# Optimization experiments

Hardware: AMD Instinct MI355X
Metric: run time of the kernel (lower is better)

## Reference

```python
import jax, jax.numpy as jnp
import numpy as np

N = 50000
E = 800000
NODE_SIZE = 64
NUM_RADIAL = 20
CUTOFF = 5.0


def setup_inputs() -> dict:
    key = jax.random.key(0)
    ks = jax.random.split(key, 12)
    node_scalar = jax.random.normal(ks[0], (N, NODE_SIZE), dtype=jnp.float32)
    node_vector = jax.random.normal(ks[1], (N, 3, NODE_SIZE), dtype=jnp.float32)
    edge = jax.random.randint(ks[2], (E, 2), 0, N, dtype=jnp.int64)
    edge_diff = jax.random.normal(ks[3], (E, 3), dtype=jnp.float32)
    # positive distances in (0, cutoff]; most edges inside cutoff
    edge_dist = jax.random.uniform(ks[4], (E, 1), dtype=jnp.float32) * CUTOFF + 1e-2
    s = 1.0 / np.sqrt(NODE_SIZE)
    r = 1.0 / np.sqrt(NUM_RADIAL)
    W1 = jax.random.normal(ks[5], (NODE_SIZE, NODE_SIZE), dtype=jnp.float32) * s
    b1 = jnp.zeros((NODE_SIZE,), dtype=jnp.float32)
    W2 = jax.random.normal(ks[6], (NODE_SIZE, 3 * NODE_SIZE), dtype=jnp.float32) * s
    b2 = jnp.zeros((3 * NODE_SIZE,), dtype=jnp.float32)
    Wf = jax.random.normal(ks[7], (NUM_RADIAL, 3 * NODE_SIZE), dtype=jnp.float32) * r
    bf = jnp.zeros((3 * NODE_SIZE,), dtype=jnp.float32)
    return {"node_scalar": node_scalar, "node_vector": node_vector, "edge": edge,
            "edge_diff": edge_diff, "edge_dist": edge_dist,
            "W1": W1, "b1": b1, "W2": W2, "b2": b2, "Wf": Wf, "bf": bf}


def reference(node_scalar, node_vector, edge, edge_diff, edge_dist, W1, b1, W2, b2, Wf, bf):
    S = NODE_SIZE
    n_nodes = node_scalar.shape[0]
    # sinc radial basis: sin(n*pi*d/cutoff)/d, n=1..num_radial -> [E, R]
    n = jnp.arange(1, NUM_RADIAL + 1, dtype=edge_dist.dtype)
    rbf = jnp.sin(edge_dist * n * jnp.pi / CUTOFF) / edge_dist
    filter_weight = rbf @ Wf + bf                       # [E, 3S]
    # cosine cutoff, broadcast [E,1] over [E,3S]
    cut = jnp.where(edge_dist < CUTOFF,
                    0.5 * (jnp.cos(jnp.pi * edge_dist / CUTOFF) + 1.0),
                    jnp.zeros((), edge_dist.dtype))
    filter_weight = filter_weight * cut
    # scalar message MLP on nodes: Linear -> SiLU -> Linear
    scalar_out = jax.nn.silu(node_scalar @ W1 + b1) @ W2 + b2   # [N, 3S]
    src = edge[:, 1]
    dst = edge[:, 0]
    filter_out = filter_weight * scalar_out[src]        # [E, 3S]
    gate_state_vector = filter_out[:, :S]
    gate_edge_vector = filter_out[:, S:2 * S]
    message_scalar = filter_out[:, 2 * S:]
    unit = (edge_diff / edge_dist)[:, :, None]          # [E, 3, 1]
    message_vector = node_vector[src] * gate_state_vector[:, None, :] + gate_edge_vector[:, None, :] * unit  # [E,3,S]
    residual_scalar = jax.ops.segment_sum(message_scalar, dst, num_segments=n_nodes)
    residual_vector = jax.ops.segment_sum(message_vector, dst, num_segments=n_nodes)
    return node_scalar + residual_scalar, node_vector + residual_vector
```

## Files before the change

### kernel.cpp

```cpp
#include <hip/hip_runtime.h>
#include <hip/hip_bf16.h>
#include <math.h>

#define N_NODES 50000
#define N_EDGES 800000
#define NRAD 20
#define NBLK 196
#define CAP 48
#define NGRP 64
#define GSZ 782

typedef short bf16x8 __attribute__((ext_vector_type(8)));
typedef _Float16 f16x8 __attribute__((ext_vector_type(8)));
typedef float f32x4 __attribute__((ext_vector_type(4)));
typedef int i32x4 __attribute__((ext_vector_type(4)));
typedef int i32x2 __attribute__((ext_vector_type(2)));

__device__ __forceinline__ unsigned short f2b(float f) {
    union { __hip_bfloat16 h; unsigned short u; } cv;
    cv.h = __float2bfloat16(f);
    return cv.u;
}
__device__ __forceinline__ unsigned int packh2(float a, float b) {
    union { _Float16 h; unsigned short u; } A, B;
    A.h = (_Float16)a; B.h = (_Float16)b;
    return (unsigned int)A.u | ((unsigned int)B.u << 16);
}
__device__ __forceinline__ f32x4 mfma16(bf16x8 a, bf16x8 b, f32x4 c) {
    return __builtin_amdgcn_mfma_f32_16x16x32_bf16(a, b, c, 0, 0, 0);
}
__device__ __forceinline__ f32x4 mfma16h(f16x8 a, f16x8 b, f32x4 c) {
    return __builtin_amdgcn_mfma_f32_16x16x32_f16(a, b, c, 0, 0, 0);
}
__device__ __forceinline__ f32x4 mkv4(float x, float y, float z, float w) {
    f32x4 v; v[0] = x; v[1] = y; v[2] = z; v[3] = w; return v;
}
union afu { i32x4 i; f16x8 h; };

__global__ __launch_bounds__(256) void prep0_kernel(
    int* __restrict__ counts, int* __restrict__ qctr,
    const float* __restrict__ W1, const float* __restrict__ W2, const float* __restrict__ Wf,
    const float* __restrict__ bfv,
    unsigned short* __restrict__ W1t, unsigned short* __restrict__ W2t,
    unsigned int* __restrict__ Bfp) {
    int i = blockIdx.x * 256 + threadIdx.x;
    if (i < N_NODES) counts[i] = 0;
    if (i < NGRP * 32) qctr[i] = 0;
    if (i < 192 * 64) {
        int n = i >> 6, k = i & 63;
        W2t[i] = f2b(W2[k * 192 + n]);
        if (i < 64 * 64) W1t[i] = f2b(W1[k * 64 + n]);
        if (i < 768) {
            int cblk = i >> 6, l = i & 63;
            int cp = cblk * 16 + (l & 15);
            int kb = (l >> 4) * 8;
            unsigned d[4];
#pragma unroll
            for (int w = 0; w < 4; w++) {
                int k0 = kb + 2 * w, k1 = k0 + 1;
                float B0 = (k0 < 20) ? Wf[k0 * 192 + cp] : ((k0 == 20) ? bfv[cp] : 0.0f);
                float B1 = (k1 < 20) ? Wf[k1 * 192 + cp] : ((k1 == 20) ? bfv[cp] : 0.0f);
                d[w] = packh2(B0, B1);
            }
            Bfp[i * 4 + 0] = d[0];
            Bfp[i * 4 + 1] = d[1];
            Bfp[i * 4 + 2] = d[2];
            Bfp[i * 4 + 3] = d[3];
        }
    }
}

__global__ void hist_kernel(const int2* __restrict__ edge2, int* __restrict__ counts) {
    int e = blockIdx.x * blockDim.x + threadIdx.x;
    if (e < N_EDGES) atomicAdd(&counts[edge2[e].x], 1);
}

__global__ __launch_bounds__(256) void scanall_kernel(const int* __restrict__ counts,
                                                      int* __restrict__ offs,
                                                      int* __restrict__ cursors) {
    __shared__ int ss[256];
    int t = threadIdx.x, b = blockIdx.x;
    int lim = b * 256;
    int s = 0;
    for (int i = t; i < lim; i += 256) s += counts[i];
    ss[t] = s;
    __syncthreads();
    for (int k = 128; k > 0; k >>= 1) {
        if (t < k) ss[t] += ss[t + k];
        __syncthreads();
    }
    int base0 = ss[0];
    __syncthreads();
    int i = lim + t;
    int v = (i < N_NODES) ? counts[i] : 0;
    ss[t] = v;
    __syncthreads();
    for (int off = 1; off < 256; off <<= 1) {
        int u = (t >= off) ? ss[t - off] : 0;
        __syncthreads();
        ss[t] += u;
        __syncthreads();
    }
    int excl = base0 + ss[t] - v;
    if (i < N_NODES) {
        offs[i] = excl;
        cursors[i] = excl;
    }
    if (i == N_NODES - 1) offs[N_NODES] = excl + v;
}

template <int C>
__global__ __launch_bounds__(256) void bucket_kernel(
    const int2* __restrict__ edge2, const float* __restrict__ ediff,
    const float* __restrict__ edist, int* __restrict__ cursors,
    float4* __restrict__ pack) {
    int e = blockIdx.x * blockDim.x + threadIdx.x;
    if (e >= N_EDGES) return;
    i32x2 edv = __builtin_nontemporal_load((const i32x2*)&edge2[e]);
    int dst = edv[0];
    int src = edv[1];
    int slot = atomicAdd(&cursors[dst], 1);
    size_t pos;
    if (C > 0) {
        if (slot >= C) return;
        pos = (size_t)dst * C + slot;
    } else {
        pos = (size_t)slot;
    }

    float dist = __builtin_nontemporal_load(&edist[e]);
    float d0 = __builtin_nontemporal_load(&ediff[3 * e]);
    float d1 = __builtin_nontemporal_load(&ediff[3 * e + 1]);
    float d2 = __builtin_nontemporal_load(&ediff[3 * e + 2]);
    float inv = __builtin_amdgcn_rcpf(dist);
    float x = dist * (3.14159265358979323846f / 5.0f);
    float s1 = __sinf(x);
    float c1 = __cosf(x);
    float cut = (dist < 5.0f) ? 0.5f * (c1 + 1.0f) : 0.0f;
    float ic = inv * cut;
    float t2 = 2.0f * c1;
    float r[NRAD];
    float sn = s1, sp = 0.0f;
#pragma unroll
    for (int k = 0; k < NRAD; k++) {
        r[k] = sn * ic;
        float nx = t2 * sn - sp;
        sp = sn;
        sn = nx;
    }
    unsigned int rp[10];
#pragma unroll
    for (int j = 0; j < 10; j++) rp[j] = packh2(r[2 * j], r[2 * j + 1]);

    f32x4* P = (f32x4*)(pack + pos * 4);
    P[0] = mkv4(__int_as_float(src), d0 * inv, d1 * inv, d2 * inv);
    P[1] = mkv4(__uint_as_float(rp[0]), __uint_as_float(rp[1]),
                __uint_as_float(rp[2]), __uint_as_float(rp[3]));
    P[2] = mkv4(__uint_as_float(rp[4]), __uint_as_float(rp[5]),
                __uint_as_float(rp[6]), __uint_as_float(rp[7]));
    P[3] = mkv4(__uint_as_float(rp[8]), __uint_as_float(rp[9]),
                __uint_as_float(packh2(cut, 0.0f)), 0.0f);
}

__global__ __launch_bounds__(256) void node_mlp_kernel(
    const float* __restrict__ ns, const float* __restrict__ nv,
    const unsigned short* __restrict__ W1t, const float* __restrict__ b1,
    const unsigned short* __restrict__ W2t, const float* __restrict__ b2,
    unsigned short* __restrict__ snb) {
    __shared__ unsigned short LB[64 * 200];
    unsigned short* H = LB;
    unsigned short* O = LB;
    int t = threadIdx.x;
    int lane = t & 63;
    int w = t >> 6;
    int c15 = lane & 15;
    int quad = lane >> 4;
    int base = blockIdx.x * 64;

    int node = base + 16 * w + c15;
    if (node >= N_NODES) node = N_NODES - 1;

    bf16x8 a0, a1;
    {
        const float* xr = ns + (size_t)node * 64 + quad * 8;
        float4 p0 = *(const float4*)xr;
        float4 p1 = *(const float4*)(xr + 4);
        float4 p2 = *(const float4*)(xr + 32);
        float4 p3 = *(const float4*)(xr + 36);
        a0[0] = (short)f2b(p0.x); a0[1] = (short)f2b(p0.y);
        a0[2] = (short)f2b(p0.z); a0[3] = (short)f2b(p0.w);
        a0[4] = (short)f2b(p1.x); a0[5] = (short)f2b(p1.y);
        a0[6] = (short)f2b(p1.z); a0[7] = (short)f2b(p1.w);
        a1[0] = (short)f2b(p2.x); a1[1] = (short)f2b(p2.y);
        a1[2] = (short)f2b(p2.z); a1[3] = (short)f2b(p2.w);
        a1[4] = (short)f2b(p3.x); a1[5] = (short)f2b(p3.y);
        a1[6] = (short)f2b(p3.z); a1[7] = (short)f2b(p3.w);
    }

#pragma unroll
    for (int nt = 0; nt < 4; nt++) {
        float bc = b1[nt * 16 + c15];
        f32x4 acc = {bc, bc, bc, bc};
        bf16x8 w0 = *(const bf16x8*)(W1t + (nt * 16 + c15) * 64 + quad * 8);
        bf16x8 w1 = *(const bf16x8*)(W1t + (nt * 16 + c15) * 64 + 32 + quad * 8);
        acc = mfma16(a0, w0, acc);
        acc = mfma16(a1, w1, acc);
#pragma unroll
        for (int r = 0; r < 4; r++) {
            float v = acc[r];
            v = v / (1.0f + __expf(-v));
            H[(16 * w + quad * 4 + r) * 72 + nt * 16 + c15] = f2b(v);
        }
    }

    bf16x8 h0 = *(const bf16x8*)(H + (16 * w + c15) * 72 + quad * 8);
    bf16x8 h1 = *(const bf16x8*)(H + (16 * w + c15) * 72 + 32 + quad * 8);
    __syncthreads();

#pragma unroll
    for (int nt = 0; nt < 12; nt++) {
        float bc = b2[nt * 16 + c15];
        f32x4 acc = {bc, bc, bc, bc};
        bf16x8 w0 = *(const bf16x8*)(W2t + (nt * 16 + c15) * 64 + quad * 8);
        bf16x8 w1 = *(const bf16x8*)(W2t + (nt * 16 + c15) * 64 + 32 + quad * 8);
        acc = mfma16(h0, w0, acc);
        acc = mfma16(h1, w1, acc);
#pragma unroll
        for (int r = 0; r < 4; r++)
            O[(16 * w + quad * 4 + r) * 200 + nt * 16 + c15] = f2b(acc[r]);
    }
    __syncthreads();

    int nb = min(64, N_NODES - base);
    for (int idx = t; idx < nb * 64; idx += 256) {
        int row = idx >> 6, ll = idx & 63;
        unsigned short o0 = O[row * 200 + ll];
        unsigned short o1 = O[row * 200 + 64 + ll];
        unsigned short o2 = O[row * 200 + 128 + ll];
        int nd = base + row;
        float v0 = nv[(size_t)nd * 192 + ll];
        float v1 = nv[(size_t)nd * 192 + 64 + ll];
        float v2 = nv[(size_t)nd * 192 + 128 + ll];
        uint3 pkv;
        pkv.x = (unsigned int)o0 | ((unsigned int)o1 << 16);
        pkv.y = (unsigned int)o2 | ((unsigned int)f2b(v0) << 16);
        pkv.z = (unsigned int)f2b(v1) | ((unsigned int)f2b(v2) << 16);
        *(uint3*)((char*)snb + (size_t)nd * 768 + ll * 12) = pkv;
    }
}

template <int C>
__global__ __launch_bounds__(256) void gather_kernel(
    const float* __restrict__ ns, const float* __restrict__ nv,
    const unsigned int* __restrict__ Bfp,
    const unsigned short* __restrict__ snb, const int* __restrict__ offs,
    const float4* __restrict__ pack, float* __restrict__ out0, float* __restrict__ out1,
    int* __restrict__ qctr) {
    __shared__ char LSH[4096 + 12288];
    int t = threadIdx.x;
    int l = t & 63;
    int w = t >> 6;
    int c = l & 15;
    int quad = l >> 4;
    char* slab = LSH + w * 1024;
    i32x4* BfL = (i32x4*)(LSH + 4096);

    for (int j = t; j < 768; j += 256) BfL[j] = ((const i32x4*)Bfp)[j];
    __syncthreads();

    const char* packb = (const char*)pack;
    const char* snbb = (const char*)snb;

    int grp = __builtin_amdgcn_readfirstlane((int)(blockIdx.x & (NGRP - 1)));
    int gbase = grp * GSZ;
    int glim = min(gbase + GSZ, N_NODES);
    int* ctr = qctr + grp * 32;

    int tk = 0;
    if (l == 0) tk = atomicAdd(ctr, 1);
    int n = gbase + __builtin_amdgcn_readfirstlane(tk);

    while (n < glim) {
        if (l == 0) tk = atomicAdd(ctr, 1);

        int start, end;
        if (C > 0) {
            start = n * C;
            int cc = __builtin_amdgcn_readfirstlane(offs[n]);
            if (cc > C) cc = C;
            end = start + cc;
        } else {
            start = __builtin_amdgcn_readfirstlane(offs[n]);
            end = __builtin_amdgcn_readfirstlane(offs[n + 1]);
        }

        float accs[4] = {0.f, 0.f, 0.f, 0.f};
        float A0[4] = {0.f, 0.f, 0.f, 0.f};
        float A1[4] = {0.f, 0.f, 0.f, 0.f};
        float A2[4] = {0.f, 0.f, 0.f, 0.f};

        for (int cb = start; cb < end; cb += 16) {
            int cnt_t = end - cb; if (cnt_t > 16) cnt_t = 16;
            int vb = cnt_t * 64;
            {
                i32x4 sv = __builtin_nontemporal_load(
                    (const i32x4*)(packb + (size_t)(unsigned)cb * 64 + (size_t)(l * 16)));
                if (l * 16 >= vb) { sv[0] = 0; sv[1] = 0; sv[2] = 0; sv[3] = 0; }
                *(i32x4*)(slab + l * 16) = sv;
            }
            afu au;
            au.i = *(const i32x4*)(slab + c * 64 + 16 + quad * 16);
            if (quad == 3) { au.i[0] = 0; au.i[1] = 0; au.i[2] = 0; au.i[3] = 0; }
            i32x4 q[4];
#pragma unroll
            for (int r = 0; r < 4; r++)
                q[r] = *(const i32x4*)(slab + (quad * 4 + r) * 64);
            uint3 G[4][4];
#pragma unroll
            for (int r = 0; r < 4; r++) {
                const char* sp = snbb + (size_t)(unsigned)q[r][0] * 768 + c * 12;
#pragma unroll
                for (int b = 0; b < 4; b++)
                    G[b][r] = *(const uint3*)(sp + b * 192);
            }
#pragma unroll
            for (int b = 0; b < 4; b++) {
                f32x4 z = {0.f, 0.f, 0.f, 0.f};
                afu b0, b4, b8;
                b0.i = BfL[b * 64 + l];
                b4.i = BfL[(b + 4) * 64 + l];
                b8.i = BfL[(b + 8) * 64 + l];
                f32x4 D0 = mfma16h(au.h, b0.h, z);
                f32x4 D4 = mfma16h(au.h, b4.h, z);
                f32x4 D8 = mfma16h(au.h, b8.h, z);
#pragma unroll
                for (int r = 0; r < 4; r++) {
                    uint3 g = G[b][r];
                    float u0 = __int_as_float(q[r][1]);
                    float u1 = __int_as_float(q[r][2]);
                    float u2 = __int_as_float(q[r][3]);
                    float s0 = __uint_as_float(g.x << 16);
                    float s1 = __uint_as_float(g.x & 0xffff0000u);
                    float s2 = __uint_as_float(g.y << 16);
                    float v0 = __uint_as_float(g.y & 0xffff0000u);
                    float v1 = __uint_as_float(g.z << 16);
                    float v2 = __uint_as_float(g.z & 0xffff0000u);
                    float gg0 = D0[r] * s0;
                    float gg1 = D4[r] * s1;
                    accs[b] = fmaf(D8[r], s2, accs[b]);
                    A0[b] = fmaf(v0, gg0, fmaf(u0, gg1, A0[b]));
                    A1[b] = fmaf(v1, gg0, fmaf(u1, gg1, A1[b]));
                    A2[b] = fmaf(v2, gg0, fmaf(u2, gg1, A2[b]));
                }
            }
        }

#pragma unroll
        for (int b = 0; b < 4; b++) {
            accs[b] += __shfl_xor(accs[b], 16); accs[b] += __shfl_xor(accs[b], 32);
            A0[b] += __shfl_xor(A0[b], 16);     A0[b] += __shfl_xor(A0[b], 32);
            A1[b] += __shfl_xor(A1[b], 16);     A1[b] += __shfl_xor(A1[b], 32);
            A2[b] += __shfl_xor(A2[b], 16);     A2[b] += __shfl_xor(A2[b], 32);
        }
        float rs = quad == 0 ? accs[0] : quad == 1 ? accs[1] : quad == 2 ? accs[2] : accs[3];
        float r0 = quad == 0 ? A0[0] : quad == 1 ? A0[1] : quad == 2 ? A0[2] : A0[3];
        float r1 = quad == 0 ? A1[0] : quad == 1 ? A1[1] : quad == 2 ? A1[2] : A1[3];
        float r2 = quad == 0 ? A2[0] : quad == 1 ? A2[1] : quad == 2 ? A2[2] : A2[3];

        size_t b64 = (size_t)n * 64 + l, b192 = (size_t)n * 192 + l;
        __builtin_nontemporal_store(
            __builtin_nontemporal_load(ns + b64) + rs, out0 + b64);
        __builtin_nontemporal_store(
            __builtin_nontemporal_load(nv + b192) + r0, out1 + b192);
        __builtin_nontemporal_store(
            __builtin_nontemporal_load(nv + b192 + 64) + r1, out1 + b192 + 64);
        __builtin_nontemporal_store(
            __builtin_nontemporal_load(nv + b192 + 128) + r2, out1 + b192 + 128);

        n = gbase + __builtin_amdgcn_readfirstlane(tk);
    }
}

extern "C" void kernel_launch(void* const* d_in, const int* in_sizes, int n_in,
                              void* d_out, int out_size, void* d_ws, size_t ws_size,
                              hipStream_t stream) {
    const float* ns    = (const float*)d_in[0];
    const float* nv    = (const float*)d_in[1];
    const int2*  edge2 = (const int2*)d_in[2];
    const float* ediff = (const float*)d_in[3];
    const float* edist = (const float*)d_in[4];
    const float* W1    = (const float*)d_in[5];
    const float* b1    = (const float*)d_in[6];
    const float* W2    = (const float*)d_in[7];
    const float* b2    = (const float*)d_in[8];
    const float* Wf    = (const float*)d_in[9];
    const float* bfv   = (const float*)d_in[10];

    float* out0 = (float*)d_out;
    float* out1 = out0 + (size_t)N_NODES * 64;

    const size_t cap_pack = (size_t)N_NODES * CAP * 64;
    const size_t need_cap = cap_pack + (size_t)N_NODES * 768 + 8192 + 24576 + 12288 +
                            (size_t)N_NODES * 4 + 4096 + NGRP * 32 * 4;
    bool capmode = ws_size >= need_cap;

    char* wsp = (char*)d_ws;
    float4* pack = (float4*)wsp;
    wsp += capmode ? cap_pack : (size_t)N_EDGES * 64;
    unsigned short* snb = (unsigned short*)wsp;     wsp += (size_t)N_NODES * 768;
    unsigned short* W1t = (unsigned short*)wsp;     wsp += 64 * 64 * 2;
    unsigned short* W2t = (unsigned short*)wsp;     wsp += 192 * 64 * 2;
    unsigned int* Bfp = (unsigned int*)wsp;         wsp += 12288;
    int* counts  = (int*)wsp;
    int* offs    = counts + N_NODES;
    int* cursors = offs + (N_NODES + 1);
    int* qctr = capmode ? (counts + N_NODES) : (cursors + N_NODES);

    if (capmode) {
        prep0_kernel<<<NBLK, 256, 0, stream>>>(counts, qctr, W1, W2, Wf, bfv,
                                               W1t, W2t, Bfp);
        bucket_kernel<CAP><<<(N_EDGES + 255) / 256, 256, 0, stream>>>(edge2, ediff, edist,
                                                                      counts, pack);
        node_mlp_kernel<<<(N_NODES + 63) / 64, 256, 0, stream>>>(ns, nv, W1t, b1, W2t, b2,
                                                                 snb);
        gather_kernel<CAP><<<2048, 256, 0, stream>>>(ns, nv, Bfp, snb, counts, pack,
                                                     out0, out1, qctr);
    } else {
        prep0_kernel<<<NBLK, 256, 0, stream>>>(counts, qctr, W1, W2, Wf, bfv,
                                               W1t, W2t, Bfp);
        hist_kernel<<<(N_EDGES + 255) / 256, 256, 0, stream>>>(edge2, counts);
        scanall_kernel<<<NBLK, 256, 0, stream>>>(counts, offs, cursors);
        bucket_kernel<0><<<(N_EDGES + 255) / 256, 256, 0, stream>>>(edge2, ediff, edist,
                                                                    cursors, pack);
        node_mlp_kernel<<<(N_NODES + 63) / 64, 256, 0, stream>>>(ns, nv, W1t, b1, W2t, b2,
                                                                 snb);
        gather_kernel<0><<<2048, 256, 0, stream>>>(ns, nv, Bfp, snb, offs, pack,
                                                   out0, out1, qctr);
    }
}
```

Measured before the change: 312.1 us.

## Recompute radial basis in gather and merge bucket with node MLP kernel

The bucketed edge record is halved from 64 to 32 bytes by storing only dist and its reciprocal; the sinc radial basis and cosine cutoff are now recomputed per edge inside the gather loop before the MFMA. The bucket and node-MLP kernels are merged into one launch, with blocks split by index, so the two independent phases can run concurrently. This cuts write and read traffic on the pack buffer and drops one launch, at the cost of redundant per-lane trig and recurrence work in the gather kernel (each quad computes all 20 radials).

```diff
diff --git a/kernel.cpp b/kernel.cpp
--- a/kernel.cpp
+++ b/kernel.cpp
@@ -9,6 +9,7 @@
 #define CAP 48
 #define NGRP 64
 #define GSZ 782
+#define MLPB 782
 
 typedef short bf16x8 __attribute__((ext_vector_type(8)));
 typedef _Float16 f16x8 __attribute__((ext_vector_type(8)));
@@ -110,11 +111,10 @@
 }
 
 template <int C>
-__global__ __launch_bounds__(256) void bucket_kernel(
-    const int2* __restrict__ edge2, const float* __restrict__ ediff,
+__device__ __forceinline__ void bucket_body(
+    int e, const int2* __restrict__ edge2, const float* __restrict__ ediff,
     const float* __restrict__ edist, int* __restrict__ cursors,
-    float4* __restrict__ pack) {
-    int e = blockIdx.x * blockDim.x + threadIdx.x;
+    f32x4* __restrict__ pack) {
     if (e >= N_EDGES) return;
     i32x2 edv = __builtin_nontemporal_load((const i32x2*)&edge2[e]);
     int dst = edv[0];
@@ -127,55 +127,29 @@
     } else {
         pos = (size_t)slot;
     }
-
     float dist = __builtin_nontemporal_load(&edist[e]);
     float d0 = __builtin_nontemporal_load(&ediff[3 * e]);
     float d1 = __builtin_nontemporal_load(&ediff[3 * e + 1]);
     float d2 = __builtin_nontemporal_load(&ediff[3 * e + 2]);
     float inv = __builtin_amdgcn_rcpf(dist);
-    float x = dist * (3.14159265358979323846f / 5.0f);
-    float s1 = __sinf(x);
-    float c1 = __cosf(x);
-    float cut = (dist < 5.0f) ? 0.5f * (c1 + 1.0f) : 0.0f;
-    float ic = inv * cut;
-    float t2 = 2.0f * c1;
-    float r[NRAD];
-    float sn = s1, sp = 0.0f;
-#pragma unroll
-    for (int k = 0; k < NRAD; k++) {
-        r[k] = sn * ic;
-        float nx = t2 * sn - sp;
-        sp = sn;
-        sn = nx;
-    }
-    unsigned int rp[10];
-#pragma unroll
-    for (int j = 0; j < 10; j++) rp[j] = packh2(r[2 * j], r[2 * j + 1]);
-
-    f32x4* P = (f32x4*)(pack + pos * 4);
+    f32x4* P = pack + pos * 2;
     P[0] = mkv4(__int_as_float(src), d0 * inv, d1 * inv, d2 * inv);
-    P[1] = mkv4(__uint_as_float(rp[0]), __uint_as_float(rp[1]),
-                __uint_as_float(rp[2]), __uint_as_float(rp[3]));
-    P[2] = mkv4(__uint_as_float(rp[4]), __uint_as_float(rp[5]),
-                __uint_as_float(rp[6]), __uint_as_float(rp[7]));
-    P[3] = mkv4(__uint_as_float(rp[8]), __uint_as_float(rp[9]),
-                __uint_as_float(packh2(cut, 0.0f)), 0.0f);
-}
-
-__global__ __launch_bounds__(256) void node_mlp_kernel(
-    const float* __restrict__ ns, const float* __restrict__ nv,
+    P[1] = mkv4(dist, inv, 0.0f, 0.0f);
+}
+
+__device__ __forceinline__ void mlp_body(
+    int bid, int t, const float* __restrict__ ns, const float* __restrict__ nv,
     const unsigned short* __restrict__ W1t, const float* __restrict__ b1,
     const unsigned short* __restrict__ W2t, const float* __restrict__ b2,
     unsigned short* __restrict__ snb) {
     __shared__ unsigned short LB[64 * 200];
     unsigned short* H = LB;
     unsigned short* O = LB;
-    int t = threadIdx.x;
     int lane = t & 63;
     int w = t >> 6;
     int c15 = lane & 15;
     int quad = lane >> 4;
-    int base = blockIdx.x * 64;
+    int base = bid * 64;
 
     int node = base + 16 * w + c15;
     if (node >= N_NODES) node = N_NODES - 1;
@@ -250,20 +224,38 @@
 }
 
 template <int C>
+__global__ __launch_bounds__(256) void work_kernel(
+    const float* __restrict__ ns, const float* __restrict__ nv,
+    const unsigned short* __restrict__ W1t, const float* __restrict__ b1,
+    const unsigned short* __restrict__ W2t, const float* __restrict__ b2,
+    unsigned short* __restrict__ snb,
+    const int2* __restrict__ edge2, const float* __restrict__ ediff,
+    const float* __restrict__ edist, int* __restrict__ cursors,
+    f32x4* __restrict__ pack) {
+    int bid = blockIdx.x;
+    if (bid < MLPB) {
+        mlp_body(bid, threadIdx.x, ns, nv, W1t, b1, W2t, b2, snb);
+    } else {
+        int e = (bid - MLPB) * 256 + threadIdx.x;
+        bucket_body<C>(e, edge2, ediff, edist, cursors, pack);
+    }
+}
+
+template <int C>
 __global__ __launch_bounds__(256) void gather_kernel(
     const float* __restrict__ ns, const float* __restrict__ nv,
     const unsigned int* __restrict__ Bfp,
     const unsigned short* __restrict__ snb, const int* __restrict__ offs,
-    const float4* __restrict__ pack, float* __restrict__ out0, float* __restrict__ out1,
+    const f32x4* __restrict__ pack, float* __restrict__ out0, float* __restrict__ out1,
     int* __restrict__ qctr) {
-    __shared__ char LSH[4096 + 12288];
+    __shared__ char LSH[2048 + 12288];
     int t = threadIdx.x;
     int l = t & 63;
     int w = t >> 6;
     int c = l & 15;
     int quad = l >> 4;
-    char* slab = LSH + w * 1024;
-    i32x4* BfL = (i32x4*)(LSH + 4096);
+    char* slab = LSH + w * 512;
+    i32x4* BfL = (i32x4*)(LSH + 2048);
 
     for (int j = t; j < 768; j += 256) BfL[j] = ((const i32x4*)Bfp)[j];
     __syncthreads();
@@ -301,20 +293,47 @@
 
         for (int cb = start; cb < end; cb += 16) {
             int cnt_t = end - cb; if (cnt_t > 16) cnt_t = 16;
-            int vb = cnt_t * 64;
-            {
-                i32x4 sv = __builtin_nontemporal_load(
-                    (const i32x4*)(packb + (size_t)(unsigned)cb * 64 + (size_t)(l * 16)));
-                if (l * 16 >= vb) { sv[0] = 0; sv[1] = 0; sv[2] = 0; sv[3] = 0; }
+            int vb = cnt_t * 32;
+            if (l < 32) {
+                i32x4 sv = {0, 0, 0, 0};
+                if (l * 16 < vb)
+                    sv = __builtin_nontemporal_load(
+                        (const i32x4*)(packb + (size_t)(unsigned)cb * 32 + (size_t)(l * 16)));
                 *(i32x4*)(slab + l * 16) = sv;
             }
             afu au;
-            au.i = *(const i32x4*)(slab + c * 64 + 16 + quad * 16);
-            if (quad == 3) { au.i[0] = 0; au.i[1] = 0; au.i[2] = 0; au.i[3] = 0; }
+            {
+                i32x2 di = *(const i32x2*)(slab + c * 32 + 16);
+                float dist = __int_as_float(di[0]);
+                float inv = __int_as_float(di[1]);
+                float x = dist * 0.62831853071795864769f;
+                float s1 = __sinf(x);
+                float c1 = __cosf(x);
+                float cut = (dist > 0.0f && dist < 5.0f) ? 0.5f * (c1 + 1.0f) : 0.0f;
+                float ic = inv * cut;
+                float t2 = 2.0f * c1;
+                float r[NRAD];
+                float sn = s1, sp = 0.0f;
+#pragma unroll
+                for (int k = 0; k < NRAD; k++) {
+                    r[k] = sn * ic;
+                    float nx = t2 * sn - sp;
+                    sp = sn;
+                    sn = nx;
+                }
+                unsigned pw[11];
+#pragma unroll
+                for (int j = 0; j < 10; j++) pw[j] = packh2(r[2 * j], r[2 * j + 1]);
+                pw[10] = packh2(cut, 0.0f);
+                au.i[0] = (int)(quad == 0 ? pw[0] : quad == 1 ? pw[4] : quad == 2 ? pw[8] : 0u);
+                au.i[1] = (int)(quad == 0 ? pw[1] : quad == 1 ? pw[5] : quad == 2 ? pw[9] : 0u);
+                au.i[2] = (int)(quad == 0 ? pw[2] : quad == 1 ? pw[6] : quad == 2 ? pw[10] : 0u);
+                au.i[3] = (int)(quad == 0 ? pw[3] : quad == 1 ? pw[7] : 0u);
+            }
             i32x4 q[4];
 #pragma unroll
             for (int r = 0; r < 4; r++)
-                q[r] = *(const i32x4*)(slab + (quad * 4 + r) * 64);
+                q[r] = *(const i32x4*)(slab + (quad * 4 + r) * 32);
             uint3 G[4][4];
 #pragma unroll
             for (int r = 0; r < 4; r++) {
@@ -399,14 +418,14 @@
     float* out0 = (float*)d_out;
     float* out1 = out0 + (size_t)N_NODES * 64;
 
-    const size_t cap_pack = (size_t)N_NODES * CAP * 64;
+    const size_t cap_pack = (size_t)N_NODES * CAP * 32;
     const size_t need_cap = cap_pack + (size_t)N_NODES * 768 + 8192 + 24576 + 12288 +
                             (size_t)N_NODES * 4 + 4096 + NGRP * 32 * 4;
     bool capmode = ws_size >= need_cap;
 
     char* wsp = (char*)d_ws;
-    float4* pack = (float4*)wsp;
-    wsp += capmode ? cap_pack : (size_t)N_EDGES * 64;
+    f32x4* pack = (f32x4*)wsp;
+    wsp += capmode ? cap_pack : (size_t)N_EDGES * 32;
     unsigned short* snb = (unsigned short*)wsp;     wsp += (size_t)N_NODES * 768;
     unsigned short* W1t = (unsigned short*)wsp;     wsp += 64 * 64 * 2;
     unsigned short* W2t = (unsigned short*)wsp;     wsp += 192 * 64 * 2;
@@ -416,24 +435,22 @@
     int* cursors = offs + (N_NODES + 1);
     int* qctr = capmode ? (counts + N_NODES) : (cursors + N_NODES);
 
+    const int BUCB = (N_EDGES + 255) / 256;
+
     if (capmode) {
         prep0_kernel<<<NBLK, 256, 0, stream>>>(counts, qctr, W1, W2, Wf, bfv,
                                                W1t, W2t, Bfp);
-        bucket_kernel<CAP><<<(N_EDGES + 255) / 256, 256, 0, stream>>>(edge2, ediff, edist,
-                                                                      counts, pack);
-        node_mlp_kernel<<<(N_NODES + 63) / 64, 256, 0, stream>>>(ns, nv, W1t, b1, W2t, b2,
-                                                                 snb);
+        work_kernel<CAP><<<MLPB + BUCB, 256, 0, stream>>>(
+            ns, nv, W1t, b1, W2t, b2, snb, edge2, ediff, edist, counts, pack);
         gather_kernel<CAP><<<2048, 256, 0, stream>>>(ns, nv, Bfp, snb, counts, pack,
                                                      out0, out1, qctr);
     } else {
         prep0_kernel<<<NBLK, 256, 0, stream>>>(counts, qctr, W1, W2, Wf, bfv,
                                                W1t, W2t, Bfp);
-        hist_kernel<<<(N_EDGES + 255) / 256, 256, 0, stream>>>(edge2, counts);
+        hist_kernel<<<BUCB, 256, 0, stream>>>(edge2, counts);
         scanall_kernel<<<NBLK, 256, 0, stream>>>(counts, offs, cursors);
-        bucket_kernel<0><<<(N_EDGES + 255) / 256, 256, 0, stream>>>(edge2, ediff, edist,
-                                                                    cursors, pack);
-        node_mlp_kernel<<<(N_NODES + 63) / 64, 256, 0, stream>>>(ns, nv, W1t, b1, W2t, b2,
-                                                                 snb);
+        work_kernel<0><<<MLPB + BUCB, 256, 0, stream>>>(
+            ns, nv, W1t, b1, W2t, b2, snb, edge2, ediff, edist, cursors, pack);
         gather_kernel<0><<<2048, 256, 0, stream>>>(ns, nv, Bfp, snb, offs, pack,
                                                    out0, out1, qctr);
     }
```

Result: faster. 265.3 us (-15.0%).
